# Kernel optimization log

Measured on AMD Instinct MI355X. Metric: run time of the kernel, lower is better.

Reference implementation:

```python
import jax, jax.numpy as jnp
import numpy as np

GAMMA, ZETA = -0.1, 1.1
N_BITS = 4
QMAX = (1 << N_BITS) - 1  # 15
OUT, IN, D, K = 4096, 4096, 8, 4096
L = (OUT * IN) // D  # 2097152 blocks, no padding needed


def setup_inputs() -> dict:
    key = jax.random.key(0)
    k = jax.random.split(key, 7)
    x = jax.random.normal(k[0], (4, 2048, IN), jnp.float32)
    codebook = jax.random.normal(k[1], (K, D), jnp.float32)
    indices = jax.random.randint(k[2], (L,), 0, K, jnp.int32)
    base_int = jax.random.randint(k[3], (OUT, IN), 0, QMAX, jnp.int32)
    scale = jax.random.uniform(k[4], (OUT, 1), jnp.float32)
    zero = jax.random.uniform(k[5], (OUT, 1), jnp.float32)
    bias = jax.random.normal(k[6], (OUT,), jnp.float32)
    return {"x": x, "codebook": codebook, "indices": indices,
            "base_int": base_int, "scale": scale, "zero": zero, "bias": bias}


def reference(x, codebook, indices, base_int, scale, zero, bias):
    # Gather codebook blocks and rebuild alpha with the weight's shape [OUT, IN]
    alpha = codebook[indices].reshape(OUT, IN)
    # Rectified sigmoid (soft quant mode)
    r = jnp.clip(jax.nn.sigmoid(alpha) * (ZETA - GAMMA) + GAMMA, 0.0, 1.0)
    # Affine int-quant reconstruction
    q_int = jnp.clip(base_int.astype(scale.dtype) + r + zero, 0.0, float(QMAX))
    Wq = scale * (q_int - zero)  # [OUT, IN]
    # F.linear: x @ Wq^T + bias
    return jnp.einsum('bsi,oi->bso', x, Wq) + bias
```

## Files before the change

kernel.cpp:

```cpp
#include <hip/hip_runtime.h>

#define M_DIM 8192
#define N_DIM 4096
#define K_DIM 4096
#define L_BLK 2097152
#define K2 8192

typedef __attribute__((ext_vector_type(8))) short short8;
typedef __attribute__((ext_vector_type(8))) unsigned short ushort8;
typedef __attribute__((ext_vector_type(16))) float f32x16;

__device__ __forceinline__ unsigned short f2bf(float f) {
  unsigned int u = __float_as_uint(f);
  unsigned int r = (u + 0x7fffu + ((u >> 16) & 1u)) >> 16;
  return (unsigned short)r;
}

__device__ __forceinline__ void gld16(const void* g, void* l) {
  __builtin_amdgcn_global_load_lds(
      (const __attribute__((address_space(1))) void*)g,
      (__attribute__((address_space(3))) void*)l, 16, 0, 0);
}

__global__ void prep_kernel(const float* __restrict__ cb,
                            const int* __restrict__ idx,
                            const int* __restrict__ base,
                            const float* __restrict__ scale,
                            const float* __restrict__ zero,
                            const float* __restrict__ x,
                            unsigned short* __restrict__ W,
                            unsigned short* __restrict__ xb) {
  if (blockIdx.x < L_BLK / 256) {
    const int b = blockIdx.x * 256 + threadIdx.x;
    const int o = b >> 9;
    const float s = scale[o];
    const float z = zero[o];
    const int ci = idx[b];
    const float4* crow = (const float4*)(cb + (size_t)ci * 8);
    float4 c0 = crow[0], c1 = crow[1];
    const int4* brow = (const int4*)(base + (size_t)b * 8);
    int4 b0 = brow[0], b1 = brow[1];
    float a[8]  = {c0.x, c0.y, c0.z, c0.w, c1.x, c1.y, c1.z, c1.w};
    int   bi[8] = {b0.x, b0.y, b0.z, b0.w, b1.x, b1.y, b1.z, b1.w};
    union { unsigned short h[8]; ushort8 v; } u;
#pragma unroll
    for (int d = 0; d < 8; ++d) {
      float sg = 1.0f / (1.0f + __expf(-a[d]));
      float r = fminf(fmaxf(sg * 1.2f - 0.1f, 0.0f), 1.0f);
      float q = fminf(fmaxf((float)bi[d] + r + z, 0.0f), 15.0f);
      u.h[d] = f2bf(s * (q - z));
    }
    *(ushort8*)(W + (size_t)b * 8) = u.v;
  } else {
    const size_t i = (size_t)(blockIdx.x - L_BLK / 256) * 256 + threadIdx.x;
    const float4* X = (const float4*)x;
    float4 a0 = X[i * 2], a1 = X[i * 2 + 1];
    float f[8] = {a0.x, a0.y, a0.z, a0.w, a1.x, a1.y, a1.z, a1.w};
    union { unsigned short h[8]; ushort8 v; } u;
#pragma unroll
    for (int d = 0; d < 8; ++d) u.h[d] = f2bf(f[d]);
    *(ushort8*)(xb + i * 8) = u.v;
  }
}


#define VMW(N) asm volatile("s_waitcnt vmcnt(" #N ")" ::: "memory")
#define BAR __builtin_amdgcn_s_barrier()

#define RDB(BUFO) \
  _Pragma("unroll") for (int nf = 0; nf < 2; ++nf) \
  _Pragma("unroll") for (int ks = 0; ks < 4; ++ks) \
    bf[nf][ks] = *(const short8*)(lds + (BUFO) + 32768 + \
        (wn * 64 + nf * 32 + l31) * 128 + ((ks * 32 + h16) ^ swz));

#define RDA2(BUFO, MF) \
  _Pragma("unroll") for (int mi = 0; mi < 2; ++mi) \
  _Pragma("unroll") for (int ks = 0; ks < 4; ++ks) \
    af[mi][ks] = *(const short8*)(lds + (BUFO) + \
        (wm * 128 + ((MF) + mi) * 32 + l31) * 128 + ((ks * 32 + h16) ^ swz));

#define FM2(MF) do { \
  __builtin_amdgcn_s_setprio(1); \
  _Pragma("unroll") for (int ks = 0; ks < 4; ++ks) \
  _Pragma("unroll") for (int mi = 0; mi < 2; ++mi) \
  _Pragma("unroll") for (int nf = 0; nf < 2; ++nf) \
    acc[(MF) + mi][nf] = __builtin_amdgcn_mfma_f32_32x32x16_bf16( \
        af[mi][ks], bf[nf][ks], acc[(MF) + mi][nf], 0, 0, 0); \
  __builtin_amdgcn_s_setprio(0); \
} while (0)

#define ITER(CUR, NXT, T) do { \
   \
  RDB(CUR); RDA2(CUR, 0); \
  stA(NXT, 1, (T) + 1); stA(NXT, 3, (T) + 1); \
  BAR; FM2(0); BAR; \
   \
  RDA2(CUR, 2); \
  stB(CUR, 0, (T) + 2); stB(CUR, 1, (T) + 2); \
  stB(CUR, 2, (T) + 2); stB(CUR, 3, (T) + 2); \
  stA(CUR, 0, (T) + 2); stA(CUR, 2, (T) + 2); \
  VMW(6); BAR; FM2(2); BAR; \
} while (0)

__global__ __launch_bounds__(512, 2)
void gemm_bt(const unsigned short* __restrict__ A,
             const unsigned short* __restrict__ B,
             const float* __restrict__ bias,
             float* __restrict__ C) {
  __shared__ char lds[131072];
  const int tid = threadIdx.x;
  const int lane = tid & 63;
  const int w = tid >> 6;
  const int wm = w >> 2;
  const int wn = w & 3;
  const int l31 = lane & 31;
  const int h16 = (lane >> 5) * 16;
  const int swz = (l31 & 7) << 4;

  const int s = (int)blockIdx.x;
  const int wg = (s & 7) * 64 + (s >> 3);
  const int bm = wg & 31;
  const int bn = wg >> 5;

  const char* Abase = (const char*)A + (size_t)bm * 256 * K2;
  const char* Bbase = (const char*)B + (size_t)bn * 256 * K2;

  const int strow = tid >> 3;
  const int scol = ((tid & 7) * 16) ^ ((strow & 7) << 4);
  const int sdst = w * 1024;

  auto stA = [&](int bo, int c, int kt) {
    gld16(Abase + (size_t)(c * 64 + strow) * K2 + kt * 128 + scol,
          lds + bo + c * 8192 + sdst);
  };
  auto stB = [&](int bo, int c, int kt) {
    gld16(Bbase + (size_t)(c * 64 + strow) * K2 + kt * 128 + scol,
          lds + bo + 32768 + c * 8192 + sdst);
  };

  f32x16 acc[4][2] = {};
  short8 bf[2][4];
  short8 af[2][4];

  stB(0, 0, 0); stB(0, 1, 0); stB(0, 2, 0); stB(0, 3, 0);
  stA(0, 0, 0); stA(0, 1, 0); stA(0, 2, 0); stA(0, 3, 0);
  stB(65536, 0, 1); stB(65536, 1, 1); stB(65536, 2, 1); stB(65536, 3, 1);
  stA(65536, 0, 1); stA(65536, 2, 1);
  VMW(6); BAR;

  for (int tp = 0; tp < 31; ++tp) {
    ITER(0, 65536, 2 * tp);
    ITER(65536, 0, 2 * tp + 1);
  }
  RDB(0); RDA2(0, 0);
  stA(65536, 1, 63); stA(65536, 3, 63);
  BAR; FM2(0); BAR;
  RDA2(0, 2);
  VMW(0); BAR; FM2(2); BAR;
  RDB(65536); RDA2(65536, 0);
  FM2(0);
  RDA2(65536, 2);
  FM2(2);

  const int cb0 = bn * 256 + wn * 64 + l31;
  const int hr = (lane >> 5) * 2;
  float bv0 = bias[cb0];
  float bv1 = bias[cb0 + 32];
#pragma unroll
  for (int mf = 0; mf < 4; ++mf) {
#pragma unroll
    for (int r = 0; r < 16; ++r) {
      int row = bm * 256 + wm * 128 + mf * 32 + (r & 3) + 8 * (r >> 2) + 2 * hr;
      float* Crow = C + (size_t)row * N_DIM + cb0;
      Crow[0]  = acc[mf][0][r] + bv0;
      Crow[32] = acc[mf][1][r] + bv1;
    }
  }
}

extern "C" void kernel_launch(void* const* d_in, const int* in_sizes, int n_in,
                              void* d_out, int out_size, void* d_ws, size_t ws_size,
                              hipStream_t stream) {
  const float* x     = (const float*)d_in[0];
  const float* cb    = (const float*)d_in[1];
  const int*   idx   = (const int*)d_in[2];
  const int*   base  = (const int*)d_in[3];
  const float* scale = (const float*)d_in[4];
  const float* zero  = (const float*)d_in[5];
  const float* bias  = (const float*)d_in[6];
  float* out = (float*)d_out;

  unsigned short* Wq = (unsigned short*)d_ws;
  unsigned short* Xb = (unsigned short*)((char*)d_ws + (size_t)N_DIM * K_DIM * 2);

  const int prep_blocks = L_BLK / 256 + (M_DIM * K_DIM / 8) / 256;
  prep_kernel<<<prep_blocks, 256, 0, stream>>>(cb, idx, base, scale, zero, x, Wq, Xb);
  gemm_bt<<<(M_DIM / 256) * (N_DIM / 256), 512, 0, stream>>>(Xb, Wq, bias, out);
}
```

Baseline: 343.7 us.

## Split GEMM k-tile into four 32-row A phases with finer barriers

Restructures the GEMM main loop from two phases per k-tile (each reading two 32-row A fragments) into four phases reading one A fragment each. Global-to-LDS loads are spread more evenly across the phases, and the A fragment register array shrinks by half. This cuts register pressure and interleaves loads with MFMA work more finely, at the cost of twice as many barriers per tile. The epilogue row formula is rewritten in an equivalent form.

```diff
diff --git a/kernel.cpp b/kernel.cpp
--- a/kernel.cpp
+++ b/kernel.cpp
@@ -67,39 +67,39 @@
 #define VMW(N) asm volatile("s_waitcnt vmcnt(" #N ")" ::: "memory")
 #define BAR __builtin_amdgcn_s_barrier()
 
-#define RDB(BUFO) \
+#define RDB32(BUFO) \
   _Pragma("unroll") for (int nf = 0; nf < 2; ++nf) \
   _Pragma("unroll") for (int ks = 0; ks < 4; ++ks) \
     bf[nf][ks] = *(const short8*)(lds + (BUFO) + 32768 + \
         (wn * 64 + nf * 32 + l31) * 128 + ((ks * 32 + h16) ^ swz));
 
-#define RDA2(BUFO, MF) \
-  _Pragma("unroll") for (int mi = 0; mi < 2; ++mi) \
+#define RDA32(BUFO, MF) \
   _Pragma("unroll") for (int ks = 0; ks < 4; ++ks) \
-    af[mi][ks] = *(const short8*)(lds + (BUFO) + \
-        (wm * 128 + ((MF) + mi) * 32 + l31) * 128 + ((ks * 32 + h16) ^ swz));
-
-#define FM2(MF) do { \
+    af[ks] = *(const short8*)(lds + (BUFO) + \
+        (wm * 128 + (MF) * 32 + l31) * 128 + ((ks * 32 + h16) ^ swz));
+
+#define FM32(MF) do { \
   __builtin_amdgcn_s_setprio(1); \
   _Pragma("unroll") for (int ks = 0; ks < 4; ++ks) \
-  _Pragma("unroll") for (int mi = 0; mi < 2; ++mi) \
   _Pragma("unroll") for (int nf = 0; nf < 2; ++nf) \
-    acc[(MF) + mi][nf] = __builtin_amdgcn_mfma_f32_32x32x16_bf16( \
-        af[mi][ks], bf[nf][ks], acc[(MF) + mi][nf], 0, 0, 0); \
+    acc[MF][nf] = __builtin_amdgcn_mfma_f32_32x32x16_bf16( \
+        af[ks], bf[nf][ks], acc[MF][nf], 0, 0, 0); \
   __builtin_amdgcn_s_setprio(0); \
 } while (0)
 
 #define ITER(CUR, NXT, T) do { \
-   \
-  RDB(CUR); RDA2(CUR, 0); \
+   RDB32(CUR); RDA32(CUR, 0); \
   stA(NXT, 1, (T) + 1); stA(NXT, 3, (T) + 1); \
-  BAR; FM2(0); BAR; \
-   \
-  RDA2(CUR, 2); \
+  BAR; FM32(0); BAR; \
+   RDA32(CUR, 1); \
   stB(CUR, 0, (T) + 2); stB(CUR, 1, (T) + 2); \
+  BAR; FM32(1); BAR; \
+   RDA32(CUR, 2); \
   stB(CUR, 2, (T) + 2); stB(CUR, 3, (T) + 2); \
+  BAR; FM32(2); BAR; \
+   RDA32(CUR, 3); \
   stA(CUR, 0, (T) + 2); stA(CUR, 2, (T) + 2); \
-  VMW(6); BAR; FM2(2); BAR; \
+  VMW(6); BAR; FM32(3); BAR; \
 } while (0)
 
 __global__ __launch_bounds__(512, 2)
@@ -140,7 +140,7 @@
 
   f32x16 acc[4][2] = {};
   short8 bf[2][4];
-  short8 af[2][4];
+  short8 af[4];
 
   stB(0, 0, 0); stB(0, 1, 0); stB(0, 2, 0); stB(0, 3, 0);
   stA(0, 0, 0); stA(0, 1, 0); stA(0, 2, 0); stA(0, 3, 0);
@@ -152,25 +152,33 @@
     ITER(0, 65536, 2 * tp);
     ITER(65536, 0, 2 * tp + 1);
   }
-  RDB(0); RDA2(0, 0);
+  RDB32(0); RDA32(0, 0);
   stA(65536, 1, 63); stA(65536, 3, 63);
-  BAR; FM2(0); BAR;
-  RDA2(0, 2);
-  VMW(0); BAR; FM2(2); BAR;
-  RDB(65536); RDA2(65536, 0);
-  FM2(0);
-  RDA2(65536, 2);
-  FM2(2);
+  BAR; FM32(0); BAR;
+  RDA32(0, 1);
+  BAR; FM32(1); BAR;
+  RDA32(0, 2);
+  BAR; FM32(2); BAR;
+  RDA32(0, 3);
+  VMW(0); BAR; FM32(3); BAR;
+  RDB32(65536); RDA32(65536, 0);
+  FM32(0);
+  RDA32(65536, 1);
+  FM32(1);
+  RDA32(65536, 2);
+  FM32(2);
+  RDA32(65536, 3);
+  FM32(3);
 
   const int cb0 = bn * 256 + wn * 64 + l31;
-  const int hr = (lane >> 5) * 2;
+  const int h4 = (lane >> 5) * 4;
   float bv0 = bias[cb0];
   float bv1 = bias[cb0 + 32];
 #pragma unroll
   for (int mf = 0; mf < 4; ++mf) {
 #pragma unroll
     for (int r = 0; r < 16; ++r) {
-      int row = bm * 256 + wm * 128 + mf * 32 + (r & 3) + 8 * (r >> 2) + 2 * hr;
+      int row = bm * 256 + wm * 128 + mf * 32 + (r & 3) + 8 * (r >> 2) + h4;
       float* Crow = C + (size_t)row * N_DIM + cb0;
       Crow[0]  = acc[mf][0][r] + bv0;
       Crow[32] = acc[mf][1][r] + bv1;
```

Measured after the change: 328.9 us. -4.3%, faster.
